# Kernel tuning notes

Hardware: AMD Instinct MI355X
Metric: run time of the kernel (lower is better)

Reference implementation:

```python
import jax, jax.numpy as jnp
import numpy as np

B, C, N, DI, DC = 64, 32, 1152, 8, 16
ROUTINGS = 3


def squash(x, axis=-1):
    sq = jnp.sum(x * x, axis=axis, keepdims=True)
    scale = sq / (1.0 + sq) / jnp.sqrt(sq + 1e-07)
    return scale * x


def setup_inputs() -> dict:
    key = jax.random.key(0)
    k1, k2 = jax.random.split(key)
    inputs = jax.random.normal(k1, (B, N, DI), dtype=jnp.float32)
    # Xavier-uniform init for W[n_caps, n_in, d_cap, d_in]; fan computed over last two dims
    limit = float(np.sqrt(6.0 / (DC + DI)))
    W = jax.random.uniform(k2, (C, N, DC, DI), dtype=jnp.float32, minval=-limit, maxval=limit)
    return {"inputs": inputs, "W": W}


def reference(inputs, W):
    # inputs_hat[b,c,n,i] = sum_j W[c,n,i,j] * inputs[b,n,j]
    inputs_hat = jnp.einsum('cnij,bnj->bcni', W, inputs)  # [B,C,N,DC]
    b = jnp.zeros((B, C, N), dtype=inputs_hat.dtype)
    outputs = None
    for i in range(ROUTINGS):
        c = jax.nn.softmax(b, axis=1)                      # over output capsules
        s = jnp.einsum('bcn,bcni->bci', c, inputs_hat)     # weighted sum over input caps
        outputs = squash(s)                                # [B,C,DC]
        if i < ROUTINGS - 1:
            agreement = jnp.einsum('bci,bcni->bcn', outputs, inputs_hat)
            b = b + agreement
    return outputs
```

## Files before the change

### kernel.cpp

```cpp
#include <hip/hip_runtime.h>
#include <hip/hip_bf16.h>
#include <hip/hip_fp16.h>

#define B_  64
#define C_  32
#define N_  1152
#define DI_ 8
#define DC_ 16
#define STH 512

#define HCH 2
#define HSLOT 192
#define NOCT 24

#define FCH 3
#define FSLOT 128

static __device__ __forceinline__ unsigned pkh(float a, float b) {
    __half2 t = __float22half2_rn(make_float2(a, b));
    return *reinterpret_cast<unsigned*>(&t);
}
static __device__ __forceinline__ float2 uph(unsigned u) {
    __half2 h; *reinterpret_cast<unsigned*>(&h) = u;
    return __half22float2(h);
}

__global__ __launch_bounds__(STH, 2) void caps_hat(
    const float* __restrict__ X, const float* __restrict__ W,
    uint4* __restrict__ hatg, __half2* __restrict__ p1)
{
    __shared__ float wlds[HCH * 64 * 64];

    const int xcd  = blockIdx.x & 7;
    const int k    = blockIdx.x >> 3;
    const int bg   = k & 7;
    const int slot = 24 * xcd + (k >> 3);

    const int tid  = threadIdx.x;
    const int lane = tid & 63;
    const int c    = lane & 31;
    const int h    = lane >> 5;
    const int le   = 2 * c + h;
    const int sw   = c & 7;
    const int wu   = __builtin_amdgcn_readfirstlane(tid) >> 6;
    const int b    = bg * 8 + wu;

    float acc[8];
#pragma unroll
    for (int r = 0; r < 8; r++) acc[r] = 0.f;

    for (int cc = 0; cc < 3; cc++) {
        if (cc) __syncthreads();
        const int n0 = (slot + cc * HSLOT) * HCH;

#pragma unroll
        for (int G = tid; G < HCH * 1024; G += STH) {
            const int nl = G >> 10, f = (G >> 4) & 63, q = G & 15;
            const int wc = f >> 1, wh = f & 1;
            const float4 v = *(const float4*)(W + (size_t)(wc * N_ + n0 + nl) * 128 + wh * 64 + q * 4);
            *(float4*)(wlds + (nl * 64 + f) * 64 + (q ^ (wc & 7)) * 4) = v;
        }
        __syncthreads();

#pragma unroll
        for (int nl = 0; nl < HCH; nl++) {
            const float* xp = X + ((size_t)b * N_ + n0 + nl) * DI_;
            const float4 xa = *(const float4*)xp;
            const float4 xb = *(const float4*)(xp + 4);
            uint4 hq;
            const float* frag = wlds + (nl * 64 + le) * 64;
#pragma unroll
            for (int rp = 0; rp < 4; rp++) {
                const int r0 = 2 * rp, r1 = r0 + 1;
                const int pa0 = ((2 * r0) ^ sw) * 4;
                const int pb0 = pa0 ^ 4;
                const int pa1 = ((2 * r1) ^ sw) * 4;
                const int pb1 = pa1 ^ 4;
                const float4 wa0 = *(const float4*)(frag + pa0);
                const float4 wb0 = *(const float4*)(frag + pb0);
                const float4 wa1 = *(const float4*)(frag + pa1);
                const float4 wb1 = *(const float4*)(frag + pb1);
                const float hv0 = wa0.x*xa.x + wa0.y*xa.y + wa0.z*xa.z + wa0.w*xa.w
                                + wb0.x*xb.x + wb0.y*xb.y + wb0.z*xb.z + wb0.w*xb.w;
                const float hv1 = wa1.x*xa.x + wa1.y*xa.y + wa1.z*xa.z + wa1.w*xa.w
                                + wb1.x*xb.x + wb1.y*xb.y + wb1.z*xb.z + wb1.w*xb.w;
                acc[r0] += hv0;
                acc[r1] += hv1;
                (&hq.x)[rp] = pkh(hv0, hv1);
            }
            hatg[(size_t)(b * N_ + n0 + nl) * 64 + le] = hq;
        }
    }

    __half2* pout = p1 + (size_t)(bg * HSLOT + slot) * (8 * 256);
    uint4 st;
    st.x = pkh(acc[0]*0.03125f, acc[1]*0.03125f);
    st.y = pkh(acc[2]*0.03125f, acc[3]*0.03125f);
    st.z = pkh(acc[4]*0.03125f, acc[5]*0.03125f);
    st.w = pkh(acc[6]*0.03125f, acc[7]*0.03125f);
    *(uint4*)(pout + wu * 256 + le * 4) = st;
}

__global__ __launch_bounds__(STH, 2) void caps_route(
    const uint4* __restrict__ hatg, const float* __restrict__ accb,
    float* __restrict__ p2)
{
    __shared__ float red[8 * 512];
    const int xcd  = blockIdx.x & 7;
    const int rest = blockIdx.x >> 3;
    const int ug   = rest % 3;
    const int b    = rest / 3;
    const int u    = 8 * ug + xcd;
    const int tid  = threadIdx.x;
    const int w    = tid >> 6;
    const int lane = tid & 63;
    const int c    = lane & 31;
    const int h    = lane >> 5;
    const int le   = 2 * c + h;

    const float* ap = accb + (size_t)b * 512 + le * 8;
    const float4 a0 = *(const float4*)ap;
    const float4 a1 = *(const float4*)(ap + 4);

    const uint4* hb = hatg + (size_t)(b * N_ + u * 48) * 64 + le;

    uint4 v[6];
#pragma unroll
    for (int m = 0; m < 6; m++)
        v[m] = hb[(size_t)(w + 8 * m) * 64];

    float acc[8] = {0.f,0.f,0.f,0.f,0.f,0.f,0.f,0.f};
#pragma unroll
    for (int g = 0; g < 2; g++) {
        float lg[3], sm[3];
#pragma unroll
        for (int j = 0; j < 3; j++) {
            const uint4 vv = v[g * 3 + j];
            const float2 f0 = uph(vv.x);
            const float2 f1 = uph(vv.y);
            const float2 f2 = uph(vv.z);
            const float2 f3 = uph(vv.w);
            lg[j] = f0.x*a0.x + f0.y*a0.y + f1.x*a0.z + f1.y*a0.w
                  + f2.x*a1.x + f2.y*a1.y + f3.x*a1.z + f3.y*a1.w;
        }
#pragma unroll
        for (int j = 0; j < 3; j++) lg[j] += __shfl_xor(lg[j], 32, 64);
#pragma unroll
        for (int j = 0; j < 3; j++) { lg[j] = __expf(lg[j]); sm[j] = lg[j]; }
#pragma unroll
        for (int d = 16; d >= 1; d >>= 1)
#pragma unroll
            for (int j = 0; j < 3; j++) sm[j] += __shfl_xor(sm[j], d, 64);
#pragma unroll
        for (int j = 0; j < 3; j++) {
            const float sc = lg[j] * __builtin_amdgcn_rcpf(sm[j]);
            const uint4 vv = v[g * 3 + j];
            const float2 f0 = uph(vv.x);
            const float2 f1 = uph(vv.y);
            const float2 f2 = uph(vv.z);
            const float2 f3 = uph(vv.w);
            acc[0] += sc * f0.x; acc[1] += sc * f0.y;
            acc[2] += sc * f1.x; acc[3] += sc * f1.y;
            acc[4] += sc * f2.x; acc[5] += sc * f2.y;
            acc[6] += sc * f3.x; acc[7] += sc * f3.y;
        }
    }
    *(float4*)(red + w * 512 + le * 8)     = make_float4(acc[0], acc[1], acc[2], acc[3]);
    *(float4*)(red + w * 512 + le * 8 + 4) = make_float4(acc[4], acc[5], acc[6], acc[7]);
    __syncthreads();
    float vs = 0.f;
#pragma unroll
    for (int s = 0; s < 8; s++) vs += red[s * 512 + tid];
    p2[(size_t)(b * NOCT + u) * 512 + tid] = vs;
}

__global__ __launch_bounds__(512) void caps_r1(
    const __half2* __restrict__ p1, float* __restrict__ accb,
    float* __restrict__ out, int t)
{
    const int b   = blockIdx.x >> 2;
    const int q   = blockIdx.x & 3;
    const int tid = threadIdx.x;
    const int ep  = tid >> 3;
    const int p   = tid & 7;
    const int bg  = b >> 3, bl = b & 7;
    const __half2* base = p1 + (size_t)bg * HSLOT * 2048 + bl * 256 + (q * 64 + ep);
    float vx = 0.f, vy = 0.f;
#pragma unroll 8
    for (int ch = p; ch < HSLOT; ch += 8) {
        const float2 f = __half22float2(base[(size_t)ch * 2048]);
        vx += f.x; vy += f.y;
    }
    vx += __shfl_xor(vx, 1, 64);  vy += __shfl_xor(vy, 1, 64);
    vx += __shfl_xor(vx, 2, 64);  vy += __shfl_xor(vy, 2, 64);
    vx += __shfl_xor(vx, 4, 64);  vy += __shfl_xor(vy, 4, 64);
    float sq = vx * vx + vy * vy;
    sq += __shfl_xor(sq, 8, 64);
    sq += __shfl_xor(sq, 16, 64);
    sq += __shfl_xor(sq, 32, 64);
    const float scale = sq / (1.f + sq) * rsqrtf(sq + 1e-7f);
    if (p == 0) {
        const int oidx = b * 512 + q * 128 + ep * 2;
        const float ox = vx * scale, oy = vy * scale;
        if (t == 2) { out[oidx] = ox; out[oidx + 1] = oy; }
        else if (t == 0) { accb[oidx] = ox; accb[oidx + 1] = oy; }
        else { accb[oidx] += ox; accb[oidx + 1] += oy; }
    }
}

__global__ __launch_bounds__(512) void caps_r2(
    const float* __restrict__ p2, float* __restrict__ accb,
    float* __restrict__ out, int t)
{
    const int b = blockIdx.x;
    const int e = threadIdx.x;
    const float* base = p2 + (size_t)b * (NOCT * 512) + e;
    float v = 0.f;
#pragma unroll
    for (int s = 0; s < NOCT; s++) v += base[s * 512];
    float sq = v * v;
#pragma unroll
    for (int m = 1; m <= 8; m <<= 1) sq += __shfl_xor(sq, m, 64);
    const float scale = sq / (1.f + sq) * rsqrtf(sq + 1e-7f);
    const float ov = v * scale;
    const int oidx = b * 512 + e;
    if (t == 2) out[oidx] = ov;
    else        accb[oidx] += ov;
}

__global__ __launch_bounds__(STH, 2) void caps_s_fb(
    const float* __restrict__ X, const float* __restrict__ W,
    const float* __restrict__ aout, float* __restrict__ partials, int t)
{
    __shared__ float wlds[FCH * 64 * 64];
    __shared__ float xlds[FCH * 16 * 8];
    const int bg = blockIdx.x & 3, slot = blockIdx.x >> 2;
    const int tid = threadIdx.x, w = tid >> 6, lane = tid & 63;
    const int c = lane & 31, h = lane >> 5, bl0 = w * 2, sw = c & 7;
    float areg[2][8] = {};
    if (t > 0) {
#pragma unroll
        for (int bq = 0; bq < 2; bq++) {
            const float* ap = aout + (size_t)(bg * 16 + bl0 + bq) * 512 + c * 16 + h * 8;
            const float4 a0 = *(const float4*)ap; const float4 a1 = *(const float4*)(ap + 4);
            areg[bq][0]=a0.x; areg[bq][1]=a0.y; areg[bq][2]=a0.z; areg[bq][3]=a0.w;
            areg[bq][4]=a1.x; areg[bq][5]=a1.y; areg[bq][6]=a1.z; areg[bq][7]=a1.w;
        }
    }
    float acc[2][8];
#pragma unroll
    for (int bq = 0; bq < 2; bq++)
#pragma unroll
        for (int r = 0; r < 8; r++) acc[bq][r] = 0.f;
    for (int cc = 0; cc < 3; cc++) {
        if (cc) __syncthreads();
        const int n0 = (slot + cc * FSLOT) * FCH;
        for (int G = tid; G < FCH * 1024; G += STH) {
            const int nl = G >> 10, f = (G >> 4) & 63, q = G & 15;
            const int wc = f >> 1, wh = f & 1;
            const float4 v = *(const float4*)(W + (size_t)(wc * N_ + n0 + nl) * 128 + wh * 64 + q * 4);
            *(float4*)(wlds + (nl * 64 + f) * 64 + (q ^ (wc & 7)) * 4) = v;
        }
        if (tid < FCH * 32) {
            const int nl = tid >> 5, bl = (tid >> 1) & 15, qx = tid & 1;
            const float4 v = *(const float4*)(X + (size_t)((bg * 16 + bl) * N_ + n0 + nl) * DI_ + qx * 4);
            *(float4*)(xlds + (nl * 16 + bl) * 8 + qx * 4) = v;
        }
        __syncthreads();
#pragma unroll
        for (int nl = 0; nl < FCH; nl++) {
            float4 xa[2], xb[2];
#pragma unroll
            for (int bq = 0; bq < 2; bq++) {
                const float* xp = xlds + (nl * 16 + bl0 + bq) * 8;
                xa[bq] = *(const float4*)xp; xb[bq] = *(const float4*)(xp + 4);
            }
            float hat[2][8];
            const float* frag = wlds + (nl * 64 + 2 * c + h) * 64;
#pragma unroll
            for (int r = 0; r < 8; r++) {
                const int pa = ((2 * r) ^ sw) * 4; const int pb = pa ^ 4;
                const float4 wa = *(const float4*)(frag + pa);
                const float4 wb = *(const float4*)(frag + pb);
#pragma unroll
                for (int bq = 0; bq < 2; bq++)
                    hat[bq][r] = wa.x*xa[bq].x + wa.y*xa[bq].y + wa.z*xa[bq].z + wa.w*xa[bq].w
                               + wb.x*xb[bq].x + wb.y*xb[bq].y + wb.z*xb[bq].z + wb.w*xb[bq].w;
            }
#pragma unroll
            for (int bq = 0; bq < 2; bq++) {
                float softc;
                if (t > 0) {
                    float lg = hat[bq][0]*areg[bq][0] + hat[bq][1]*areg[bq][1]
                             + hat[bq][2]*areg[bq][2] + hat[bq][3]*areg[bq][3]
                             + hat[bq][4]*areg[bq][4] + hat[bq][5]*areg[bq][5]
                             + hat[bq][6]*areg[bq][6] + hat[bq][7]*areg[bq][7];
                    lg += __shfl_xor(lg, 32, 64);
                    const float e = __expf(lg);
                    float s = e;
#pragma unroll
                    for (int m = 16; m >= 1; m >>= 1) s += __shfl_xor(s, m, 64);
                    softc = e / s;
                } else softc = 1.0f / 32.0f;
#pragma unroll
                for (int r = 0; r < 8; r++) acc[bq][r] += softc * hat[bq][r];
            }
        }
    }
    float* pout = partials + (size_t)(bg * FSLOT + slot) * (16 * 512);
#pragma unroll
    for (int bq = 0; bq < 2; bq++) {
        float* pb = pout + (bl0 + bq) * 512 + c * 16 + h * 8;
        *(float4*)pb       = make_float4(acc[bq][0], acc[bq][1], acc[bq][2], acc[bq][3]);
        *(float4*)(pb + 4) = make_float4(acc[bq][4], acc[bq][5], acc[bq][6], acc[bq][7]);
    }
}

__global__ __launch_bounds__(256) void caps_r1_fb(
    const float* __restrict__ partials, float* __restrict__ accb,
    float* __restrict__ out, int t)
{
    const int b   = blockIdx.x >> 2;
    const int q   = blockIdx.x & 3;
    const int tid = threadIdx.x;
    const int e   = q * 128 + (tid >> 1);
    const int p   = tid & 1;
    const int bg  = b >> 4, bl = b & 15;
    const float* base = partials + (size_t)bg * FSLOT * 8192 + (size_t)bl * 512 + e;
    float v = 0.f;
#pragma unroll 8
    for (int ch = p; ch < FSLOT; ch += 2)
        v += base[(size_t)ch * 8192];
    v += __shfl_xor(v, 1, 64);
    float sq = v * v;
#pragma unroll
    for (int m = 2; m <= 16; m <<= 1) sq += __shfl_xor(sq, m, 64);
    const float scale = sq / (1.f + sq) * rsqrtf(sq + 1e-7f);
    const float ov = v * scale;
    if (p == 0) {
        const int oidx = b * 512 + e;
        if (t == 2) out[oidx] = ov;
        else        accb[oidx] = (t == 0) ? ov : (accb[oidx] + ov);
    }
}

extern "C" void kernel_launch(void* const* d_in, const int* in_sizes, int n_in,
                              void* d_out, int out_size, void* d_ws, size_t ws_size,
                              hipStream_t stream) {
    const float* X = (const float*)d_in[0];
    const float* W = (const float*)d_in[1];
    float* out = (float*)d_out;

    const size_t hat_b = (size_t)B_ * N_ * 512 * 2;
    const size_t p1_b  = (size_t)8 * HSLOT * 2048 * 4;
    const size_t p2_b  = (size_t)B_ * NOCT * 512 * 4;
    const size_t acc_b = (size_t)B_ * 512 * 4;

    if (ws_size >= hat_b + p1_b + p2_b + acc_b) {
        char* ws = (char*)d_ws;
        uint4*   hatg = (uint4*)ws;
        __half2* p1   = (__half2*)(ws + hat_b);
        float*   p2   = (float*)(ws + hat_b + p1_b);
        float*   accb = (float*)(ws + hat_b + p1_b + p2_b);
        caps_hat  <<<1536, STH, 0, stream>>>(X, W, hatg, p1);
        caps_r1   <<<256, 512, 0, stream>>>(p1, accb, out, 0);
        caps_route<<<B_ * NOCT, STH, 0, stream>>>(hatg, accb, p2);
        caps_r2   <<<64, 512, 0, stream>>>(p2, accb, out, 1);
        caps_route<<<B_ * NOCT, STH, 0, stream>>>(hatg, accb, p2);
        caps_r2   <<<64, 512, 0, stream>>>(p2, accb, out, 2);
    } else {
        float* partials = (float*)d_ws;
        float* accb = partials + (size_t)512 * 8192;
        for (int t = 0; t < 3; t++) {
            caps_s_fb<<<512, STH, 0, stream>>>(X, W, accb, partials, t);
            caps_r1_fb<<<256, 256, 0, stream>>>(partials, accb, out, t);
        }
    }
}
```

Before: 129.7 us.

## Drop in-block LDS reduction in routing kernel and widen partial-sum reduction

Each wavefront in the routing kernel now owns a contiguous group of 6 input capsules and writes its own partial sum straight to global memory, replacing the shared-memory reduction across 8 wavefronts and the block barrier. The number of partials per batch grows from 24 to 192, so the follow-up reduction kernel is spread over 4x more blocks, with 4 lanes per element combined by shuffles. This removes LDS traffic and synchronisation and drops the XCD-aware block mapping. In exchange, partial-sum writes and reads grow 8x.

New measurement: 145.1 us. 1.12x slower.

```diff
diff --git a/kernel.cpp b/kernel.cpp
--- a/kernel.cpp
+++ b/kernel.cpp
@@ -11,7 +11,7 @@
 
 #define HCH 2
 #define HSLOT 192
-#define NOCT 24
+#define NU  192
 
 #define FCH 3
 #define FSLOT 128
@@ -105,14 +105,11 @@
     const uint4* __restrict__ hatg, const float* __restrict__ accb,
     float* __restrict__ p2)
 {
-    __shared__ float red[8 * 512];
-    const int xcd  = blockIdx.x & 7;
-    const int rest = blockIdx.x >> 3;
-    const int ug   = rest % 3;
-    const int b    = rest / 3;
-    const int u    = 8 * ug + xcd;
     const int tid  = threadIdx.x;
-    const int w    = tid >> 6;
+    const int wu   = __builtin_amdgcn_readfirstlane(tid) >> 6;
+    const int gw   = blockIdx.x * 8 + wu;
+    const int b    = gw / NU;
+    const int u    = gw % NU;
     const int lane = tid & 63;
     const int c    = lane & 31;
     const int h    = lane >> 5;
@@ -122,12 +119,12 @@
     const float4 a0 = *(const float4*)ap;
     const float4 a1 = *(const float4*)(ap + 4);
 
-    const uint4* hb = hatg + (size_t)(b * N_ + u * 48) * 64 + le;
+    const uint4* hb = hatg + (size_t)(b * N_ + u * 6) * 64 + le;
 
     uint4 v[6];
 #pragma unroll
     for (int m = 0; m < 6; m++)
-        v[m] = hb[(size_t)(w + 8 * m) * 64];
+        v[m] = hb[(size_t)m * 64];
 
     float acc[8] = {0.f,0.f,0.f,0.f,0.f,0.f,0.f,0.f};
 #pragma unroll
@@ -165,13 +162,9 @@
             acc[6] += sc * f3.x; acc[7] += sc * f3.y;
         }
     }
-    *(float4*)(red + w * 512 + le * 8)     = make_float4(acc[0], acc[1], acc[2], acc[3]);
-    *(float4*)(red + w * 512 + le * 8 + 4) = make_float4(acc[4], acc[5], acc[6], acc[7]);
-    __syncthreads();
-    float vs = 0.f;
-#pragma unroll
-    for (int s = 0; s < 8; s++) vs += red[s * 512 + tid];
-    p2[(size_t)(b * NOCT + u) * 512 + tid] = vs;
+    float* pb = p2 + ((size_t)b * NU + u) * 512 + le * 8;
+    *(float4*)pb       = make_float4(acc[0], acc[1], acc[2], acc[3]);
+    *(float4*)(pb + 4) = make_float4(acc[4], acc[5], acc[6], acc[7]);
 }
 
 __global__ __launch_bounds__(512) void caps_r1(
@@ -212,20 +205,30 @@
     const float* __restrict__ p2, float* __restrict__ accb,
     float* __restrict__ out, int t)
 {
-    const int b = blockIdx.x;
-    const int e = threadIdx.x;
-    const float* base = p2 + (size_t)b * (NOCT * 512) + e;
+    const int b   = blockIdx.x >> 2;
+    const int q   = blockIdx.x & 3;
+    const int tid = threadIdx.x;
+    const int e   = q * 128 + (tid >> 2);
+    const int p   = tid & 3;
+    const float* base = p2 + (size_t)b * (NU * 512) + e;
     float v = 0.f;
-#pragma unroll
-    for (int s = 0; s < NOCT; s++) v += base[s * 512];
+#pragma unroll 8
+    for (int s = p; s < NU; s += 4)
+        v += base[(size_t)s * 512];
+    v += __shfl_xor(v, 1, 64);
+    v += __shfl_xor(v, 2, 64);
     float sq = v * v;
-#pragma unroll
-    for (int m = 1; m <= 8; m <<= 1) sq += __shfl_xor(sq, m, 64);
+    sq += __shfl_xor(sq, 4, 64);
+    sq += __shfl_xor(sq, 8, 64);
+    sq += __shfl_xor(sq, 16, 64);
+    sq += __shfl_xor(sq, 32, 64);
     const float scale = sq / (1.f + sq) * rsqrtf(sq + 1e-7f);
     const float ov = v * scale;
-    const int oidx = b * 512 + e;
-    if (t == 2) out[oidx] = ov;
-    else        accb[oidx] += ov;
+    if (p == 0) {
+        const int oidx = b * 512 + e;
+        if (t == 2) out[oidx] = ov;
+        else        accb[oidx] += ov;
+    }
 }
 
 __global__ __launch_bounds__(STH, 2) void caps_s_fb(
@@ -353,7 +356,7 @@
 
     const size_t hat_b = (size_t)B_ * N_ * 512 * 2;
     const size_t p1_b  = (size_t)8 * HSLOT * 2048 * 4;
-    const size_t p2_b  = (size_t)B_ * NOCT * 512 * 4;
+    const size_t p2_b  = (size_t)B_ * NU * 512 * 4;
     const size_t acc_b = (size_t)B_ * 512 * 4;
 
     if (ws_size >= hat_b + p1_b + p2_b + acc_b) {
@@ -364,10 +367,10 @@
         float*   accb = (float*)(ws + hat_b + p1_b + p2_b);
         caps_hat  <<<1536, STH, 0, stream>>>(X, W, hatg, p1);
         caps_r1   <<<256, 512, 0, stream>>>(p1, accb, out, 0);
-        caps_route<<<B_ * NOCT, STH, 0, stream>>>(hatg, accb, p2);
-        caps_r2   <<<64, 512, 0, stream>>>(p2, accb, out, 1);
-        caps_route<<<B_ * NOCT, STH, 0, stream>>>(hatg, accb, p2);
-        caps_r2   <<<64, 512, 0, stream>>>(p2, accb, out, 2);
+        caps_route<<<(B_ * NU) / 8, STH, 0, stream>>>(hatg, accb, p2);
+        caps_r2   <<<256, 512, 0, stream>>>(p2, accb, out, 1);
+        caps_route<<<(B_ * NU) / 8, STH, 0, stream>>>(hatg, accb, p2);
+        caps_r2   <<<256, 512, 0, stream>>>(p2, accb, out, 2);
     } else {
         float* partials = (float*)d_ws;
         float* accb = partials + (size_t)512 * 8192;
```
